# Performance work log

Hardware: AMD Instinct MI355X
Metric: run time of the kernel (lower is better)

The kernel has to match this reference:

```python
import jax, jax.numpy as jnp
import numpy as np

N = 100000      # nodes (categories_nums[0])
E = 1600000     # edges
FEAT = 16       # features_num
HID = 32        # hidden
IDE = 16        # id_embed_size
EMB = 8         # embed_size
CAT_MAX = 1000  # categorical vocab (categories_nums[1:])
K = 3           # TAGConv hops (sparse=False)
NC = 2          # num_class
IN_DIM = IDE + 2 * EMB + HID  # 64 -> TAGConv input
EPS = 1e-5


def layer_norm(x, g, b):
    m = jnp.mean(x, axis=-1, keepdims=True)
    v = jnp.mean((x - m) ** 2, axis=-1, keepdims=True)
    return (x - m) * jax.lax.rsqrt(v + EPS) * g + b


def setup_inputs() -> dict:
    key = jax.random.key(0)
    ks = jax.random.split(key, 20)
    s = 0.05
    return {
        "x": jax.random.normal(ks[0], (N, FEAT), jnp.float32),
        "edge_index": jax.random.randint(ks[1], (2, E), 0, N, jnp.int64),
        "edge_weight": jax.random.uniform(ks[2], (E,), jnp.float32),
        "categories_value": jax.random.randint(ks[3], (N, 3), 0, CAT_MAX, jnp.int64),
        "id_table": jax.random.normal(ks[4], (N, IDE), jnp.float32) * s,
        "lin0_id_W": jax.random.normal(ks[5], (IDE, IDE), jnp.float32) * s,
        "lin0_id_b": jnp.zeros((IDE,), jnp.float32),
        "emb1": jax.random.normal(ks[6], (CAT_MAX, EMB), jnp.float32) * s,
        "emb2": jax.random.normal(ks[7], (CAT_MAX, EMB), jnp.float32) * s,
        "lin0_emb_W": jax.random.normal(ks[8], (2 * EMB, 2 * EMB), jnp.float32) * s,
        "lin0_emb_b": jnp.zeros((2 * EMB,), jnp.float32),
        "lin0_W": jax.random.normal(ks[9], (FEAT, HID), jnp.float32) * s,
        "lin0_b": jnp.zeros((HID,), jnp.float32),
        "ln0_g": jnp.ones((IN_DIM,), jnp.float32),
        "ln0_b": jnp.zeros((IN_DIM,), jnp.float32),
        "tag_W": jax.random.normal(ks[10], (K + 1, IN_DIM, HID), jnp.float32) * s,
        "tag_b": jnp.zeros((HID,), jnp.float32),
        "ln1_g": jnp.ones((HID,), jnp.float32),
        "ln1_b": jnp.zeros((HID,), jnp.float32),
        "lin1_W": jax.random.normal(ks[11], (HID, NC), jnp.float32) * s,
        "lin1_b": jnp.zeros((NC,), jnp.float32),
    }


def reference(x, edge_index, edge_weight, categories_value, id_table, lin0_id_W,
              lin0_id_b, emb1, emb2, lin0_emb_W, lin0_emb_b, lin0_W, lin0_b,
              ln0_g, ln0_b, tag_W, tag_b, ln1_g, ln1_b, lin1_W, lin1_b):
    # eval mode: dropouts are identity
    h = jax.nn.elu(x @ lin0_W + lin0_b)                       # [N, HID]
    ide = id_table[categories_value[:, 0]]                    # [N, IDE]
    ide = jax.nn.elu(ide @ lin0_id_W + lin0_id_b)
    er = jnp.concatenate([emb1[categories_value[:, 1]],
                          emb2[categories_value[:, 2]]], axis=1)  # [N, 2*EMB]
    er = jax.nn.elu(er @ lin0_emb_W + lin0_emb_b)
    feat = jnp.concatenate([ide, h, er], axis=1)              # [N, IN_DIM]
    feat = layer_norm(feat, ln0_g, ln0_b)

    # TAGConv: gcn_norm without self-loops, K-hop propagation
    row, col = edge_index[0], edge_index[1]                   # source -> target
    deg = jax.ops.segment_sum(edge_weight, col, num_segments=N)
    dis = jnp.where(deg > 0, deg ** -0.5, 0.0)
    norm = dis[row] * edge_weight * dis[col]                  # [E]

    out = feat @ tag_W[0]                                     # [N, HID]
    xk = feat
    for k in range(1, K + 1):
        xk = jax.ops.segment_sum(xk[row] * norm[:, None], col, num_segments=N)
        out = out + xk @ tag_W[k]
    out = out + tag_b

    out = jax.nn.relu(out)
    out = layer_norm(out, ln1_g, ln1_b)
    out = out @ lin1_W + lin1_b                               # [N, NC]
    return jax.nn.log_softmax(out, axis=-1)
```

## Files before the change

kernel.cpp:

```cpp
#include <hip/hip_runtime.h>
#include <hip/hip_bf16.h>

typedef unsigned short u16;
typedef unsigned int   u32;
typedef unsigned long long u64;
typedef u32 u32x2 __attribute__((ext_vector_type(2)));

#define FIX_SCALE 16777216.0f
#define FIX_INV   (1.0f / 16777216.0f)
#define CNT_SHIFT 40
#define DEG_MASK  ((1ULL << CNT_SHIFT) - 1)

__device__ __forceinline__ float b2f(u16 u) { return __uint_as_float(((u32)u) << 16); }
__device__ __forceinline__ u16 f2b(float f) {
    u32 u = __float_as_uint(f);
    return (u16)((u + 0x7FFFu + ((u >> 16) & 1u)) >> 16);
}
__device__ __forceinline__ float elu(float v) { return v > 0.f ? v : expm1f(v); }
__device__ __forceinline__ float ldf(const void* p, size_t i, int f32) {
    return f32 ? ((const float*)p)[i] : b2f(((const u16*)p)[i]);
}
__device__ __forceinline__ float plo(u32 a) { return __uint_as_float(a << 16); }
__device__ __forceinline__ float phi(u32 a) { return __uint_as_float(a & 0xFFFF0000u); }

__global__ void k_flags(const u32* __restrict__ gw, const int* __restrict__ ei,
                        const int* __restrict__ cat, int* __restrict__ flags) {
    if (threadIdx.x == 0 && blockIdx.x == 0) {
        flags[0] = (gw[0] == 0x3F800000u) ? 1 : 0;
        flags[1] = ((ei[1]  | ei[3]  | ei[5]  | ei[7])  == 0) ? 2 : 1;
        flags[2] = ((cat[1] | cat[3] | cat[5] | cat[7]) == 0) ? 2 : 1;
    }
}

__global__ __launch_bounds__(256) void k_feathist(
    const void* __restrict__ x, const int* __restrict__ cat,
    const void* __restrict__ id_table, const void* __restrict__ W_id, const void* __restrict__ b_id,
    const void* __restrict__ emb1, const void* __restrict__ emb2,
    const void* __restrict__ W_emb, const void* __restrict__ b_emb,
    const void* __restrict__ W0, const void* __restrict__ b0,
    const void* __restrict__ g0, const void* __restrict__ bb0,
    const void* __restrict__ tagW0,
    u32* __restrict__ feat, float* __restrict__ out_acc,
    const int* __restrict__ ei, const void* __restrict__ ew,
    u64* __restrict__ packed, u16* __restrict__ rank,
    const int* __restrict__ flags, int N, int E, int nbN)
{
    __shared__ float sW0[512];
    __shared__ float sb0[32];
    __shared__ float sWid[256];
    __shared__ float sbid[16];
    __shared__ float sWe[256];
    __shared__ float sbe[16];
    __shared__ float sg[64], sb[64];
    __shared__ float sT0t[2048];
    int tid = threadIdx.x;
    int f32 = flags[0], s = flags[1], cs = flags[2];

    int e = blockIdx.x * 256 + tid;
    u64 old = 0;
    bool hist = (e < E);
    if (hist) {
        const int* colp = ei + (size_t)E * s;
        int cdst = colp[(size_t)e * s];
        float w = ldf(ew, e, f32);
        u64 add = (1ULL << CNT_SHIFT) | (u64)(w * FIX_SCALE + 0.5f);
        old = atomicAdd(&packed[cdst], add);
    }

    if (blockIdx.x < nbN) {
        for (int i = tid; i < 512; i += 256) sW0[i] = ldf(W0, i, f32);
        if (tid < 32) sb0[tid] = ldf(b0, tid, f32);
        sWid[tid] = ldf(W_id, tid, f32);
        if (tid < 16) sbid[tid] = ldf(b_id, tid, f32);
        sWe[tid] = ldf(W_emb, tid, f32);
        if (tid < 16) sbe[tid] = ldf(b_emb, tid, f32);
        if (tid < 64) { sg[tid] = ldf(g0, tid, f32); sb[tid] = ldf(bb0, tid, f32); }
        for (int i = tid; i < 2048; i += 256) {
            int j = i >> 6, d = i & 63;
            sT0t[i] = ldf(tagW0, (size_t)d * 32 + j, f32);
        }
        __syncthreads();

        int i = blockIdx.x * 256 + tid;
        if (i < N) {
            size_t cb = (size_t)i * 3 * cs;
            int c0 = cat[cb], c1 = cat[cb + cs], c2 = cat[cb + 2 * cs];
            float f[64];
            {
                float t[16];
                #pragma unroll
                for (int q = 0; q < 16; q++) t[q] = ldf(id_table, (size_t)c0 * 16 + q, f32);
                #pragma unroll
                for (int j = 0; j < 16; j++) {
                    float a = sbid[j];
                    #pragma unroll
                    for (int ff = 0; ff < 16; ff++) a += t[ff] * sWid[ff * 16 + j];
                    f[j] = elu(a);
                }
            }
            {
                float t[16];
                #pragma unroll
                for (int q = 0; q < 16; q++) t[q] = ldf(x, (size_t)i * 16 + q, f32);
                #pragma unroll
                for (int j = 0; j < 32; j++) {
                    float a = sb0[j];
                    #pragma unroll
                    for (int ff = 0; ff < 16; ff++) a += t[ff] * sW0[ff * 32 + j];
                    f[16 + j] = elu(a);
                }
            }
            {
                float t[16];
                #pragma unroll
                for (int q = 0; q < 8; q++) t[q] = ldf(emb1, (size_t)c1 * 8 + q, f32);
                #pragma unroll
                for (int q = 0; q < 8; q++) t[8 + q] = ldf(emb2, (size_t)c2 * 8 + q, f32);
                #pragma unroll
                for (int j = 0; j < 16; j++) {
                    float a = sbe[j];
                    #pragma unroll
                    for (int ff = 0; ff < 16; ff++) a += t[ff] * sWe[ff * 16 + j];
                    f[48 + j] = elu(a);
                }
            }
            float m = 0.f;
            #pragma unroll
            for (int d = 0; d < 64; d++) m += f[d];
            m *= (1.f / 64.f);
            float var = 0.f;
            #pragma unroll
            for (int d = 0; d < 64; d++) { float df = f[d] - m; var += df * df; }
            var *= (1.f / 64.f);
            float rs = rsqrtf(var + 1e-5f);
            #pragma unroll
            for (int d = 0; d < 64; d++) f[d] = (f[d] - m) * rs * sg[d] + sb[d];

            u32* fp = feat + (size_t)i * 32;
            #pragma unroll
            for (int q = 0; q < 32; q++) fp[q] = ((u32)f2b(f[2 * q + 1]) << 16) | f2b(f[2 * q]);

            float* oa = out_acc + (size_t)i * 32;
            for (int j = 0; j < 32; j++) {
                float a = 0.f;
                #pragma unroll
                for (int d = 0; d < 64; d++) a += f[d] * sT0t[j * 64 + d];
                oa[j] = a;
            }
        }
    }
    if (hist) rank[e] = (u16)(old >> CNT_SHIFT);
}

__global__ __launch_bounds__(256) void k_scan1(const u64* __restrict__ packed, int* __restrict__ ebuf,
                                               int* __restrict__ bsum, float* __restrict__ dis, int N)
{
    __shared__ int sdat[256];
    int tid = threadIdx.x;
    int i = blockIdx.x * 256 + tid;
    u64 pv = (i < N) ? packed[i] : 0ULL;
    int v = (int)(pv >> CNT_SHIFT);
    sdat[tid] = v;
    __syncthreads();
    for (int off = 1; off < 256; off <<= 1) {
        int t = (tid >= off) ? sdat[tid - off] : 0;
        __syncthreads();
        sdat[tid] += t;
        __syncthreads();
    }
    if (i < N) {
        ebuf[i] = sdat[tid] - v;
        u64 db = pv & DEG_MASK;
        dis[i] = db ? rsqrtf((float)db * FIX_INV) : 0.f;
    }
    if (tid == 255) bsum[blockIdx.x] = sdat[255];
}

__global__ __launch_bounds__(512) void k_scan2(const int* __restrict__ bsum, int* __restrict__ boff, int NB)
{
    __shared__ int sdat[512];
    __shared__ int scarry;
    int tid = threadIdx.x;
    if (tid == 0) scarry = 0;
    __syncthreads();
    for (int base = 0; base < NB; base += 512) {
        int i = base + tid;
        int v = (i < NB) ? bsum[i] : 0;
        sdat[tid] = v;
        __syncthreads();
        for (int off = 1; off < 512; off <<= 1) {
            int t = (tid >= off) ? sdat[tid - off] : 0;
            __syncthreads();
            sdat[tid] += t;
            __syncthreads();
        }
        if (i < NB) boff[i] = scarry + sdat[tid] - v;
        __syncthreads();
        if (tid == 0) scarry += sdat[511];
        __syncthreads();
    }
}

__global__ __launch_bounds__(256) void k_scan3(const int* __restrict__ ebuf, const int* __restrict__ boff,
                                               int* __restrict__ rowptr, int N, int E)
{
    int i = blockIdx.x * 256 + threadIdx.x;
    if (i >= N) return;
    rowptr[i] = boff[blockIdx.x] + ebuf[i];
    if (i == N - 1) rowptr[N] = E;
}

__global__ __launch_bounds__(256) void k_scatter(const int* __restrict__ ei, const void* __restrict__ ew,
                                                 const float* __restrict__ dis, const u16* __restrict__ rank,
                                                 const int* __restrict__ rowptr, int2* __restrict__ csr,
                                                 const int* __restrict__ flags, int E)
{
    int f32 = flags[0], s = flags[1];
    const int* row = ei;
    const int* col = ei + (size_t)E * s;
    int e = blockIdx.x * 256 + threadIdx.x;
    if (e >= E) return;
    int r = row[(size_t)e * s], c = col[(size_t)e * s];
    float nrm = dis[r] * ldf(ew, e, f32) * dis[c];
    csr[rowptr[c] + (int)rank[e]] = make_int2(r, __float_as_int(nrm));
}

template<int FOLD>
__global__ __launch_bounds__(256) void k_hop(
    const u32* __restrict__ fin, u32* __restrict__ fout, float* __restrict__ oacc,
    const int* __restrict__ rowptr, const int2* __restrict__ csr,
    const void* __restrict__ tagW, const int* __restrict__ flags, int N, int k)
{
    __shared__ float sT[FOLD ? 2048 : 1];
    if (FOLD) {
        int f32 = flags[0];
        size_t tb = (size_t)k * 2048;
        for (int i = threadIdx.x; i < 2048; i += 256) sT[i] = ldf(tagW, tb + i, f32);
        __syncthreads();
    }
    int tid = threadIdx.x;
    int node = blockIdx.x * 4 + (tid >> 6);
    if (node >= N) return;
    int lane = tid & 63;
    int g = (lane >> 4) & 3;
    int c = lane & 15;
    int start = rowptr[node], end = rowptr[node + 1];

    const u32x2* fin2 = (const u32x2*)fin;
    float v0 = 0.f, v1 = 0.f, v2 = 0.f, v3 = 0.f;
    int e = start;
    for (; e + 8 <= end; e += 8) {
        int2 ma = csr[e + g];
        int2 mb = csr[e + 4 + g];
        u32x2 aa = fin2[(size_t)(u32)ma.x * 16 + c];
        u32x2 ab = fin2[(size_t)(u32)mb.x * 16 + c];
        float wa = __int_as_float(ma.y), wb = __int_as_float(mb.y);
        v0 += plo(aa.x) * wa; v1 += phi(aa.x) * wa; v2 += plo(aa.y) * wa; v3 += phi(aa.y) * wa;
        v0 += plo(ab.x) * wb; v1 += phi(ab.x) * wb; v2 += plo(ab.y) * wb; v3 += phi(ab.y) * wb;
    }
    for (; e < end; e += 4) {
        int ee = e + g;
        int2 m = make_int2(0, 0);
        if (ee < end) m = csr[ee];
        u32x2 a = fin2[(size_t)(u32)m.x * 16 + c];
        float w = __int_as_float(m.y);
        v0 += plo(a.x) * w; v1 += phi(a.x) * w; v2 += plo(a.y) * w; v3 += phi(a.y) * w;
    }
    v0 += __shfl_xor(v0, 16); v1 += __shfl_xor(v1, 16); v2 += __shfl_xor(v2, 16); v3 += __shfl_xor(v3, 16);
    v0 += __shfl_xor(v0, 32); v1 += __shfl_xor(v1, 32); v2 += __shfl_xor(v2, 32); v3 += __shfl_xor(v3, 32);

    if (lane < 16) {
        u32x2 pw;
        pw.x = ((u32)f2b(v1) << 16) | f2b(v0);
        pw.y = ((u32)f2b(v3) << 16) | f2b(v2);
        ((u32x2*)fout)[(size_t)node * 16 + c] = pw;
    }

    if (FOLD) {
        int col = lane & 31, h = lane >> 5;
        float acc = 0.f;
        #pragma unroll
        for (int q = 0; q < 8; q++) {
            int csrc = h * 8 + q;
            int d0 = csrc * 4;
            float b0 = __shfl(v0, csrc);
            float b1 = __shfl(v1, csrc);
            float b2 = __shfl(v2, csrc);
            float b3 = __shfl(v3, csrc);
            acc += b0 * sT[(d0 + 0) * 32 + col] + b1 * sT[(d0 + 1) * 32 + col]
                 + b2 * sT[(d0 + 2) * 32 + col] + b3 * sT[(d0 + 3) * 32 + col];
        }
        acc += __shfl_xor(acc, 32);
        if (h == 0) oacc[(size_t)node * 32 + col] += acc;
    }
}

__global__ __launch_bounds__(256) void k_head(
    const float* __restrict__ oacc, const u32* __restrict__ x2b, const u32* __restrict__ x3b,
    const void* __restrict__ tagW, const void* __restrict__ tag_b,
    const void* __restrict__ g1, const void* __restrict__ b1,
    const void* __restrict__ W1, const void* __restrict__ bb1,
    void* __restrict__ out, const int* __restrict__ flags, int N)
{
    __shared__ float sT2t[2048], sT3t[2048];
    __shared__ float stb[32], sg[32], sbb[32], sW1[64], sb1v[2];
    int tid = threadIdx.x;
    int f32 = flags[0];
    for (int i = tid; i < 2048; i += 256) {
        int j = i >> 6, d = i & 63;
        sT2t[i] = ldf(tagW, (size_t)2 * 2048 + (size_t)d * 32 + j, f32);
        sT3t[i] = ldf(tagW, (size_t)3 * 2048 + (size_t)d * 32 + j, f32);
    }
    if (tid < 32) { stb[tid] = ldf(tag_b, tid, f32); sg[tid] = ldf(g1, tid, f32); sbb[tid] = ldf(b1, tid, f32); }
    if (tid < 64) sW1[tid] = ldf(W1, tid, f32);
    if (tid < 2) sb1v[tid] = ldf(bb1, tid, f32);
    __syncthreads();

    int i = blockIdx.x * 256 + tid;
    if (i >= N) return;

    float acc[32];
    const float4* oa4 = (const float4*)(oacc + (size_t)i * 32);
    #pragma unroll
    for (int q = 0; q < 8; q++) {
        float4 t = oa4[q];
        acc[4 * q] = t.x; acc[4 * q + 1] = t.y; acc[4 * q + 2] = t.z; acc[4 * q + 3] = t.w;
    }
    float xv[64];
    {
        const u32* p = x2b + (size_t)i * 32;
        #pragma unroll
        for (int q = 0; q < 32; q++) { u32 a = p[q]; xv[2 * q] = plo(a); xv[2 * q + 1] = phi(a); }
        for (int j = 0; j < 32; j++) {
            float a = 0.f;
            #pragma unroll
            for (int d = 0; d < 64; d++) a += xv[d] * sT2t[j * 64 + d];
            acc[j] += a;
        }
    }
    {
        const u32* p = x3b + (size_t)i * 32;
        #pragma unroll
        for (int q = 0; q < 32; q++) { u32 a = p[q]; xv[2 * q] = plo(a); xv[2 * q + 1] = phi(a); }
        for (int j = 0; j < 32; j++) {
            float a = 0.f;
            #pragma unroll
            for (int d = 0; d < 64; d++) a += xv[d] * sT3t[j * 64 + d];
            acc[j] += a;
        }
    }
    float o[32]; float m = 0.f;
    #pragma unroll
    for (int j = 0; j < 32; j++) { float t = acc[j] + stb[j]; t = t > 0.f ? t : 0.f; o[j] = t; m += t; }
    m *= (1.f / 32.f);
    float var = 0.f;
    #pragma unroll
    for (int j = 0; j < 32; j++) { float d = o[j] - m; var += d * d; }
    var *= (1.f / 32.f);
    float rs = rsqrtf(var + 1e-5f);
    float z0 = sb1v[0], z1 = sb1v[1];
    #pragma unroll
    for (int j = 0; j < 32; j++) {
        float t = (o[j] - m) * rs * sg[j] + sbb[j];
        z0 += t * sW1[2 * j];
        z1 += t * sW1[2 * j + 1];
    }
    float mx = fmaxf(z0, z1);
    float l = mx + logf(expf(z0 - mx) + expf(z1 - mx));
    if (f32) {
        ((float*)out)[(size_t)i * 2]     = z0 - l;
        ((float*)out)[(size_t)i * 2 + 1] = z1 - l;
    } else {
        *((u32*)((u16*)out + (size_t)i * 2)) = ((u32)f2b(z1 - l) << 16) | f2b(z0 - l);
    }
}

extern "C" void kernel_launch(void* const* d_in, const int* in_sizes, int n_in,
                              void* d_out, int out_size, void* d_ws, size_t ws_size,
                              hipStream_t stream)
{
    const void* x        = d_in[0];
    const int*  ei       = (const int*)d_in[1];
    const void* ew       = d_in[2];
    const int*  cat      = (const int*)d_in[3];
    const void* id_table = d_in[4];
    const void* W_id     = d_in[5];
    const void* b_id     = d_in[6];
    const void* emb1     = d_in[7];
    const void* emb2     = d_in[8];
    const void* W_emb    = d_in[9];
    const void* b_emb    = d_in[10];
    const void* W0       = d_in[11];
    const void* b0       = d_in[12];
    const void* g0       = d_in[13];
    const void* bb0      = d_in[14];
    const void* tagW     = d_in[15];
    const void* tag_b    = d_in[16];
    const void* g1       = d_in[17];
    const void* b1       = d_in[18];
    const void* W1       = d_in[19];
    const void* bb1      = d_in[20];

    int N = in_sizes[0] / 16;
    int E = in_sizes[2];
    int nb = (N + 255) / 256;
    int eb = (E + 255) / 256;

    char* ws = (char*)d_ws;
    size_t off = 0;
    int*   flags  = (int*)(ws + off);   off += 256;
    float* oacc   = (float*)(ws + off); off += (size_t)N * 32 * 4;
    u32*   featA  = (u32*)(ws + off);   off += (size_t)N * 32 * 4;
    u32*   f1     = (u32*)(ws + off);   off += (size_t)N * 32 * 4;
    int2*  csr    = (int2*)(ws + off);  off += (size_t)E * 8;
    int*   rowptr = (int*)(ws + off);   off += ((size_t)N + 1) * 4;
    off = (off + 255) & ~(size_t)255;
    u16*   rank   = (u16*)(ws + off);   off += (size_t)E * 2;
    off = (off + 255) & ~(size_t)255;
    u64*   packed = (u64*)(ws + off);   off += (size_t)N * 8;
    int*   ebuf   = (int*)(ws + off);   off += (size_t)N * 4;
    float* dis    = (float*)(ws + off); off += (size_t)N * 4;
    int*   bsum   = (int*)(ws + off);   off += (size_t)nb * 4;
    int*   boff   = (int*)(ws + off);   off += (size_t)nb * 4;

    hipMemsetAsync(packed, 0, (size_t)N * 8, stream);
    k_flags<<<1, 64, 0, stream>>>((const u32*)g0, ei, cat, flags);

    k_feathist<<<eb, 256, 0, stream>>>(x, cat, id_table, W_id, b_id, emb1, emb2, W_emb, b_emb,
                                       W0, b0, g0, bb0, tagW, featA, oacc,
                                       ei, ew, packed, rank, flags, N, E, nb);
    k_scan1<<<nb, 256, 0, stream>>>(packed, ebuf, bsum, dis, N);
    k_scan2<<<1, 512, 0, stream>>>(bsum, boff, nb);
    k_scan3<<<nb, 256, 0, stream>>>(ebuf, boff, rowptr, N, E);
    k_scatter<<<eb, 256, 0, stream>>>(ei, ew, dis, rank, rowptr, csr, flags, E);

    int hb = (N + 3) / 4;
    k_hop<1><<<hb, 256, 0, stream>>>(featA, f1, oacc, rowptr, csr, tagW, flags, N, 1);
    k_hop<0><<<hb, 256, 0, stream>>>(f1, featA, oacc, rowptr, csr, tagW, flags, N, 2);
    k_hop<0><<<hb, 256, 0, stream>>>(featA, f1, oacc, rowptr, csr, tagW, flags, N, 3);
    k_head<<<nb, 256, 0, stream>>>(oacc, featA, f1, tagW, tag_b, g1, b1, W1, bb1,
                                   d_out, flags, N);
}
```

Measured before the change: 437.9 us.

## Widen hop gathers to 16-byte loads and process two edges per histogram thread

The hop kernel now has each lane load 16 bytes (8 bf16 features) per neighbor, so eight lanes cover a row and eight edges are in flight per wavefront step instead of four, with the reduction and fold adjusted to match. The feature/histogram kernel handles two edges per thread with half the blocks, which lowers the block count for the edge-histogram part. Wider loads aim to cut memory instructions and raise memory-level parallelism in the gather, at the cost of more registers and an extra shuffle stage. nbN still bounds node blocks, and with 1.6M edges there are still enough blocks to cover all nodes.

Measured after the change: 434.0 us. Within noise of the previous version (-0.9%).

```diff
diff --git a/kernel.cpp b/kernel.cpp
--- a/kernel.cpp
+++ b/kernel.cpp
@@ -5,6 +5,7 @@
 typedef unsigned int   u32;
 typedef unsigned long long u64;
 typedef u32 u32x2 __attribute__((ext_vector_type(2)));
+typedef u32 u32x4 __attribute__((ext_vector_type(4)));
 
 #define FIX_SCALE 16777216.0f
 #define FIX_INV   (1.0f / 16777216.0f)
@@ -56,15 +57,20 @@
     int tid = threadIdx.x;
     int f32 = flags[0], s = flags[1], cs = flags[2];
 
-    int e = blockIdx.x * 256 + tid;
-    u64 old = 0;
-    bool hist = (e < E);
-    if (hist) {
-        const int* colp = ei + (size_t)E * s;
-        int cdst = colp[(size_t)e * s];
-        float w = ldf(ew, e, f32);
-        u64 add = (1ULL << CNT_SHIFT) | (u64)(w * FIX_SCALE + 0.5f);
-        old = atomicAdd(&packed[cdst], add);
+    int e0 = blockIdx.x * 512 + tid;
+    int e1 = e0 + 256;
+    u64 old0 = 0, old1 = 0;
+    bool h0 = (e0 < E), h1 = (e1 < E);
+    const int* colp = ei + (size_t)E * s;
+    if (h0) {
+        int cdst = colp[(size_t)e0 * s];
+        float w = ldf(ew, e0, f32);
+        old0 = atomicAdd(&packed[cdst], (1ULL << CNT_SHIFT) | (u64)(w * FIX_SCALE + 0.5f));
+    }
+    if (h1) {
+        int cdst = colp[(size_t)e1 * s];
+        float w = ldf(ew, e1, f32);
+        old1 = atomicAdd(&packed[cdst], (1ULL << CNT_SHIFT) | (u64)(w * FIX_SCALE + 0.5f));
     }
 
     if (blockIdx.x < nbN) {
@@ -149,7 +155,8 @@
             }
         }
     }
-    if (hist) rank[e] = (u16)(old >> CNT_SHIFT);
+    if (h0) rank[e0] = (u16)(old0 >> CNT_SHIFT);
+    if (h1) rank[e1] = (u16)(old1 >> CNT_SHIFT);
 }
 
 __global__ __launch_bounds__(256) void k_scan1(const u64* __restrict__ packed, int* __restrict__ ebuf,
@@ -242,53 +249,68 @@
     int node = blockIdx.x * 4 + (tid >> 6);
     if (node >= N) return;
     int lane = tid & 63;
-    int g = (lane >> 4) & 3;
-    int c = lane & 15;
+    int o = (lane >> 3) & 7;
+    int c = lane & 7;
     int start = rowptr[node], end = rowptr[node + 1];
 
-    const u32x2* fin2 = (const u32x2*)fin;
+    const u32x4* fin4 = (const u32x4*)fin;
     float v0 = 0.f, v1 = 0.f, v2 = 0.f, v3 = 0.f;
+    float v4 = 0.f, v5 = 0.f, v6 = 0.f, v7 = 0.f;
     int e = start;
-    for (; e + 8 <= end; e += 8) {
-        int2 ma = csr[e + g];
-        int2 mb = csr[e + 4 + g];
-        u32x2 aa = fin2[(size_t)(u32)ma.x * 16 + c];
-        u32x2 ab = fin2[(size_t)(u32)mb.x * 16 + c];
+    for (; e + 16 <= end; e += 16) {
+        int2 ma = csr[e + o];
+        int2 mb = csr[e + 8 + o];
+        u32x4 aa = fin4[(size_t)(u32)ma.x * 8 + c];
+        u32x4 ab = fin4[(size_t)(u32)mb.x * 8 + c];
         float wa = __int_as_float(ma.y), wb = __int_as_float(mb.y);
         v0 += plo(aa.x) * wa; v1 += phi(aa.x) * wa; v2 += plo(aa.y) * wa; v3 += phi(aa.y) * wa;
+        v4 += plo(aa.z) * wa; v5 += phi(aa.z) * wa; v6 += plo(aa.w) * wa; v7 += phi(aa.w) * wa;
         v0 += plo(ab.x) * wb; v1 += phi(ab.x) * wb; v2 += plo(ab.y) * wb; v3 += phi(ab.y) * wb;
-    }
-    for (; e < end; e += 4) {
-        int ee = e + g;
-        int2 m = make_int2(0, 0);
-        if (ee < end) m = csr[ee];
-        u32x2 a = fin2[(size_t)(u32)m.x * 16 + c];
+        v4 += plo(ab.z) * wb; v5 += phi(ab.z) * wb; v6 += plo(ab.w) * wb; v7 += phi(ab.w) * wb;
+    }
+    for (; e < end; e += 8) {
+        int ee = e + o;
+        int2 m = (ee < end) ? csr[ee] : make_int2(0, 0);
+        u32x4 a = fin4[(size_t)(u32)m.x * 8 + c];
         float w = __int_as_float(m.y);
         v0 += plo(a.x) * w; v1 += phi(a.x) * w; v2 += plo(a.y) * w; v3 += phi(a.y) * w;
-    }
+        v4 += plo(a.z) * w; v5 += phi(a.z) * w; v6 += plo(a.w) * w; v7 += phi(a.w) * w;
+    }
+    v0 += __shfl_xor(v0, 8);  v1 += __shfl_xor(v1, 8);  v2 += __shfl_xor(v2, 8);  v3 += __shfl_xor(v3, 8);
+    v4 += __shfl_xor(v4, 8);  v5 += __shfl_xor(v5, 8);  v6 += __shfl_xor(v6, 8);  v7 += __shfl_xor(v7, 8);
     v0 += __shfl_xor(v0, 16); v1 += __shfl_xor(v1, 16); v2 += __shfl_xor(v2, 16); v3 += __shfl_xor(v3, 16);
+    v4 += __shfl_xor(v4, 16); v5 += __shfl_xor(v5, 16); v6 += __shfl_xor(v6, 16); v7 += __shfl_xor(v7, 16);
     v0 += __shfl_xor(v0, 32); v1 += __shfl_xor(v1, 32); v2 += __shfl_xor(v2, 32); v3 += __shfl_xor(v3, 32);
-
-    if (lane < 16) {
-        u32x2 pw;
+    v4 += __shfl_xor(v4, 32); v5 += __shfl_xor(v5, 32); v6 += __shfl_xor(v6, 32); v7 += __shfl_xor(v7, 32);
+
+    if (lane < 8) {
+        u32x4 pw;
         pw.x = ((u32)f2b(v1) << 16) | f2b(v0);
         pw.y = ((u32)f2b(v3) << 16) | f2b(v2);
-        ((u32x2*)fout)[(size_t)node * 16 + c] = pw;
+        pw.z = ((u32)f2b(v5) << 16) | f2b(v4);
+        pw.w = ((u32)f2b(v7) << 16) | f2b(v6);
+        ((u32x4*)fout)[(size_t)node * 8 + lane] = pw;
     }
 
     if (FOLD) {
         int col = lane & 31, h = lane >> 5;
         float acc = 0.f;
         #pragma unroll
-        for (int q = 0; q < 8; q++) {
-            int csrc = h * 8 + q;
-            int d0 = csrc * 4;
+        for (int q = 0; q < 4; q++) {
+            int csrc = h * 4 + q;
+            int d0 = csrc * 8;
             float b0 = __shfl(v0, csrc);
             float b1 = __shfl(v1, csrc);
             float b2 = __shfl(v2, csrc);
             float b3 = __shfl(v3, csrc);
+            float b4 = __shfl(v4, csrc);
+            float b5 = __shfl(v5, csrc);
+            float b6 = __shfl(v6, csrc);
+            float b7 = __shfl(v7, csrc);
             acc += b0 * sT[(d0 + 0) * 32 + col] + b1 * sT[(d0 + 1) * 32 + col]
-                 + b2 * sT[(d0 + 2) * 32 + col] + b3 * sT[(d0 + 3) * 32 + col];
+                 + b2 * sT[(d0 + 2) * 32 + col] + b3 * sT[(d0 + 3) * 32 + col]
+                 + b4 * sT[(d0 + 4) * 32 + col] + b5 * sT[(d0 + 5) * 32 + col]
+                 + b6 * sT[(d0 + 6) * 32 + col] + b7 * sT[(d0 + 7) * 32 + col];
         }
         acc += __shfl_xor(acc, 32);
         if (h == 0) oacc[(size_t)node * 32 + col] += acc;
@@ -405,6 +427,7 @@
     int E = in_sizes[2];
     int nb = (N + 255) / 256;
     int eb = (E + 255) / 256;
+    int eb2 = (E + 511) / 512;
 
     char* ws = (char*)d_ws;
     size_t off = 0;
@@ -426,9 +449,9 @@
     hipMemsetAsync(packed, 0, (size_t)N * 8, stream);
     k_flags<<<1, 64, 0, stream>>>((const u32*)g0, ei, cat, flags);
 
-    k_feathist<<<eb, 256, 0, stream>>>(x, cat, id_table, W_id, b_id, emb1, emb2, W_emb, b_emb,
-                                       W0, b0, g0, bb0, tagW, featA, oacc,
-                                       ei, ew, packed, rank, flags, N, E, nb);
+    k_feathist<<<eb2, 256, 0, stream>>>(x, cat, id_table, W_id, b_id, emb1, emb2, W_emb, b_emb,
+                                        W0, b0, g0, bb0, tagW, featA, oacc,
+                                        ei, ew, packed, rank, flags, N, E, nb);
     k_scan1<<<nb, 256, 0, stream>>>(packed, ebuf, bsum, dis, N);
     k_scan2<<<1, 512, 0, stream>>>(bsum, boff, nb);
     k_scan3<<<nb, 256, 0, stream>>>(ebuf, boff, rowptr, N, E);
```
